# Optimization experiments

Hardware: AMD Instinct MI355X
Metric: run time of the kernel (lower is better)

## Reference

```python
import jax, jax.numpy as jnp
import numpy as np

N_HEAD = 16


def _rope_cos_sin(T, head_dim, dtype):
    inv_freq = 1.0 / (10000.0 ** (jnp.arange(0, head_dim, 2, dtype=jnp.float32) / head_dim))
    t = jnp.arange(T, dtype=jnp.float32)
    freqs = jnp.outer(t, inv_freq)  # [T, head_dim//2]
    return jnp.cos(freqs).astype(dtype), jnp.sin(freqs).astype(dtype)


def _apply_rope(x, cos, sin):
    # x: [B, H, T, D]; cos/sin: [T, D//2]
    x_even = x[..., ::2]
    x_odd = x[..., 1::2]
    c = cos[None, None, :, :]
    s = sin[None, None, :, :]
    out_even = x_even * c - x_odd * s
    out_odd = x_even * s + x_odd * c
    # interleave back: [..., D//2, 2] -> [..., D]
    return jnp.stack((out_even, out_odd), axis=-1).reshape(x.shape)


def setup_inputs() -> dict:
    key = jax.random.key(0)
    k1, k2, k3 = jax.random.split(key, 3)
    B, T, C = 2, 2048, 1024
    x = jax.random.normal(k1, (B, T, C), dtype=jnp.float32)
    w_qkv = jax.random.normal(k2, (C, 3 * C), dtype=jnp.float32) * (1.0 / np.sqrt(C))
    w_proj = jax.random.normal(k3, (C, C), dtype=jnp.float32) * (1.0 / np.sqrt(C))
    b_proj = jnp.zeros((C,), dtype=jnp.float32)
    return {"x": x, "w_qkv": w_qkv, "w_proj": w_proj, "b_proj": b_proj}


def reference(x, w_qkv, w_proj, b_proj):
    B, T, C = x.shape
    H = N_HEAD
    D = C // H
    qkv = x @ w_qkv  # [B, T, 3C]
    q, k, v = jnp.split(qkv, 3, axis=2)
    # [B, T, C] -> [B, H, T, D]
    q = q.reshape(B, T, H, D).transpose(0, 2, 1, 3)
    k = k.reshape(B, T, H, D).transpose(0, 2, 1, 3)
    v = v.reshape(B, T, H, D).transpose(0, 2, 1, 3)
    cos, sin = _rope_cos_sin(T, D, q.dtype)
    q = _apply_rope(q, cos, sin)
    k = _apply_rope(k, cos, sin)
    # causal SDPA
    scale = 1.0 / np.sqrt(D)
    att = jnp.einsum('bhqd,bhkd->bhqk', q, k) * scale
    causal = jnp.tril(jnp.ones((T, T), dtype=bool))
    att = jnp.where(causal[None, None, :, :], att, jnp.finfo(att.dtype).min)
    att = jax.nn.softmax(att, axis=-1)
    y = jnp.einsum('bhqk,bhkd->bhqd', att, v)  # [B, H, T, D]
    y = y.transpose(0, 2, 1, 3).reshape(B, T, C)
    return y @ w_proj + b_proj
```

## Files before the change

### kernel.cpp

```cpp
#include <hip/hip_runtime.h>
#include <math.h>

#define T_SEQ 2048
#define CDIM  1024
#define HEADS 16
#define DHEAD 64
#define BATCH 2
#define M_ROWS 4096
#define QSCALE 0.18033688011112042f

typedef unsigned short u16;
typedef unsigned int u32;
typedef __attribute__((ext_vector_type(8))) short bf16x8;
typedef __attribute__((ext_vector_type(4))) float f32x4;

__device__ inline u16 f2bf(float f) {
    u32 u = __builtin_bit_cast(u32, f);
    u32 r = (u + 0x7fffu + ((u >> 16) & 1u)) >> 16;
    return (u16)r;
}

__device__ inline u32 cvtpk(float lo, float hi) {
    u32 r;
    asm("v_cvt_pk_bf16_f32 %0, %1, %2" : "=v"(r) : "v"(lo), "v"(hi));
    return r;
}

__device__ inline float fexp2(float x) {
#if __has_builtin(__builtin_amdgcn_exp2f)
    return __builtin_amdgcn_exp2f(x);
#else
    float r; asm("v_exp_f32 %0, %1" : "=v"(r) : "v"(x)); return r;
#endif
}

__device__ inline void gload16(const void* g, void* l) {
    __builtin_amdgcn_global_load_lds(
        (const __attribute__((address_space(1))) void*)g,
        (__attribute__((address_space(3))) void*)l, 16, 0, 0);
}

__global__ void rope_table_kernel(float* __restrict__ cosT, float* __restrict__ sinT) {
    int idx = blockIdx.x * blockDim.x + threadIdx.x;
    if (idx >= T_SEQ * 32) return;
    int t = idx >> 5;
    int i = idx & 31;
    float expo = (2.0f * (float)i) / 64.0f;
    float inv = powf(10000.0f, -expo);
    float a = (float)t * inv;
    cosT[idx] = cosf(a);
    sinT[idx] = sinf(a);
}

__global__ __launch_bounds__(256)
void conv_bf16(const float* __restrict__ in, u16* __restrict__ out, int n8) {
    int i = blockIdx.x * blockDim.x + threadIdx.x;
    if (i >= n8) return;
    const float4* p = (const float4*)(in + (size_t)i * 8);
    float4 a = p[0], b = p[1];
    uint4 o;
    o.x = (u32)f2bf(a.x) | ((u32)f2bf(a.y) << 16);
    o.y = (u32)f2bf(a.z) | ((u32)f2bf(a.w) << 16);
    o.z = (u32)f2bf(b.x) | ((u32)f2bf(b.y) << 16);
    o.w = (u32)f2bf(b.z) | ((u32)f2bf(b.w) << 16);
    *(uint4*)(out + (size_t)i * 8) = o;
}

__global__ __launch_bounds__(256)
void convT64(const float* __restrict__ in, u16* __restrict__ out, int K, int N) {
    __shared__ float Ls[64][65];
    const int tid = threadIdx.x;
    const int k0 = blockIdx.y << 6, n0 = blockIdx.x << 6;
    const int r0 = tid >> 4, c4 = (tid & 15) << 2;
#pragma unroll
    for (int p = 0; p < 4; p++) {
        int r = r0 + (p << 4);
        float4 v = *(const float4*)&in[(size_t)(k0 + r) * N + n0 + c4];
        Ls[r][c4 + 0] = v.x; Ls[r][c4 + 1] = v.y;
        Ls[r][c4 + 2] = v.z; Ls[r][c4 + 3] = v.w;
    }
    __syncthreads();
    const int n = tid >> 2, kq = (tid & 3) << 4;
    u32 pk[8];
#pragma unroll
    for (int j = 0; j < 8; j++) {
        float lo = Ls[kq + 2 * j][n], hi = Ls[kq + 2 * j + 1][n];
        pk[j] = (u32)f2bf(lo) | ((u32)f2bf(hi) << 16);
    }
    u32* dst = (u32*)&out[(size_t)(n0 + n) * K + k0 + kq];
    ((uint4*)dst)[0] = make_uint4(pk[0], pk[1], pk[2], pk[3]);
    ((uint4*)dst)[1] = make_uint4(pk[4], pk[5], pk[6], pk[7]);
}

__global__ __launch_bounds__(256)
void transposeV(const u16* __restrict__ in, u16* __restrict__ out) {
    __shared__ u16 Ls[64][72];
    const int tid = threadIdx.x;
    const int bh = blockIdx.y;
    const int t0 = blockIdx.x << 6;
    const u16* src = in + ((size_t)bh << 17) + ((size_t)t0 << 6);
#pragma unroll
    for (int p = 0; p < 2; p++) {
        int L = tid + (p << 8);
        int t = L >> 3, c = L & 7;
        uint4 v = *(const uint4*)&src[(size_t)t * 64 + (c << 3)];
        *(uint4*)&Ls[t][c << 3] = v;
    }
    __syncthreads();
    const int d = tid >> 2, tq = (tid & 3) << 4;
    u32 pk[8];
#pragma unroll
    for (int j = 0; j < 8; j++) {
        u16 lo = Ls[tq + 2 * j][d], hi = Ls[tq + 2 * j + 1][d];
        pk[j] = (u32)lo | ((u32)hi << 16);
    }
    u16* dst = out + ((size_t)bh << 17) + ((size_t)d << 11) + t0 + tq;
    ((uint4*)dst)[0] = make_uint4(pk[0], pk[1], pk[2], pk[3]);
    ((uint4*)dst)[1] = make_uint4(pk[4], pk[5], pk[6], pk[7]);
}

template <int EPI>
__global__ __launch_bounds__(256)
void gemm_bf16(const u16* __restrict__ A, const u16* __restrict__ Bt,
               int N, int K,
               const float* __restrict__ bias, float* __restrict__ outF,
               u16* __restrict__ qOut, u16* __restrict__ kOut, u16* __restrict__ vOut,
               const float* __restrict__ cosT, const float* __restrict__ sinT) {
    __shared__ u16 Alds[2][128 * 32];
    __shared__ u16 Blds[2][128 * 32];
    const int tid = threadIdx.x;
    const int lane = tid & 63;
    const int w = tid >> 6;
    const int wr = w >> 1, wc = w & 1;
    const int g = lane >> 4, l15 = lane & 15;
    const int m0 = blockIdx.y * 128, n0 = blockIdx.x * 128;

    f32x4 acc[4][4];
#pragma unroll
    for (int m = 0; m < 4; m++)
#pragma unroll
        for (int n = 0; n < 4; n++)
#pragma unroll
            for (int e = 0; e < 4; e++) acc[m][n][e] = 0.f;

    int aoff[4], boff[4];
#pragma unroll
    for (int m = 0; m < 4; m++) {
        aoff[m] = ((wr << 6) + (m << 4) + l15) * 64 + (g << 4);
        boff[m] = ((wc << 6) + (m << 4) + l15) * 64 + (g << 4);
    }
    const int rowA0 = tid >> 2, kk0 = (tid & 3) << 3;

#define GSTAGE(BUF, K0)                                                          \
    {                                                                            \
        _Pragma("unroll") for (int pq = 0; pq < 2; pq++) {                       \
            int L = tid + (pq << 8);                                             \
            int row = rowA0 + (pq << 6);                                         \
            gload16(A + (size_t)(m0 + row) * K + (K0) + kk0, &Alds[BUF][0] + L * 8); \
            gload16(Bt + (size_t)(n0 + row) * K + (K0) + kk0, &Blds[BUF][0] + L * 8); \
        }                                                                        \
    }

    GSTAGE(0, 0);
    const int nt = K >> 5;
    int cur = 0;
    for (int t = 0; t < nt; t++) {
        if (t + 1 < nt) {
            GSTAGE(cur ^ 1, ((t + 1) << 5));
            asm volatile("s_waitcnt vmcnt(4)" ::: "memory");
        } else {
            asm volatile("s_waitcnt vmcnt(0)" ::: "memory");
        }
        __builtin_amdgcn_s_barrier();
        asm volatile("" ::: "memory");
        bf16x8 af[4], bfr[4];
#pragma unroll
        for (int m = 0; m < 4; m++) af[m] = *(const bf16x8*)((const char*)&Alds[cur][0] + aoff[m]);
#pragma unroll
        for (int n = 0; n < 4; n++) bfr[n] = *(const bf16x8*)((const char*)&Blds[cur][0] + boff[n]);
#pragma unroll
        for (int m = 0; m < 4; m++)
#pragma unroll
            for (int n = 0; n < 4; n++)
                acc[m][n] = __builtin_amdgcn_mfma_f32_16x16x32_bf16(af[m], bfr[n], acc[m][n], 0, 0, 0);
        asm volatile("" ::: "memory");
        __builtin_amdgcn_s_barrier();
        cur ^= 1;
    }
#undef GSTAGE

    if (EPI == 0) {
        const int sec = n0 >> 10;
#pragma unroll
        for (int m = 0; m < 4; m++) {
#pragma unroll
            for (int j = 0; j < 4; j++) {
                int t = m0 + (wr << 6) + (m << 4) + (g << 2) + j;
                int b = t >> 11, tt = t & 2047;
#pragma unroll
                for (int n = 0; n < 4; n++) {
                    int cc = (n0 + (wc << 6) + (n << 4) + l15) & 1023;
                    int h = cc >> 6, d = cc & 63;
                    float val = acc[m][n][j];
                    float o = val;
                    if (sec < 2) {
                        float partner = __shfl_xor(val, 1);
                        int i0 = d >> 1;
                        float c = cosT[tt * 32 + i0], s = sinT[tt * 32 + i0];
                        o = ((d & 1) == 0) ? (val * c - partner * s)
                                           : (partner * s + val * c);
                        if (sec == 0) o *= QSCALE;
                    }
                    size_t off = (((size_t)((b * 16 + h) * 2048 + tt)) << 6) + d;
                    u16* dst = (sec == 0) ? qOut : ((sec == 1) ? kOut : vOut);
                    dst[off] = f2bf(o);
                }
            }
        }
    } else {
#pragma unroll
        for (int m = 0; m < 4; m++) {
#pragma unroll
            for (int j = 0; j < 4; j++) {
                int t = m0 + (wr << 6) + (m << 4) + (g << 2) + j;
#pragma unroll
                for (int n = 0; n < 4; n++) {
                    int col = n0 + (wc << 6) + (n << 4) + l15;
                    outF[(size_t)t * N + col] = acc[m][n][j] + bias[col];
                }
            }
        }
    }
}

__device__ __forceinline__ void kv_stage(const u16* Kbase, const u16* Vtbase,
                                         u16* Kl, u16* Vl, int tid, int kt) {
#pragma unroll
    for (int pp = 0; pp < 2; pp++) {
        int L = tid + (pp << 8);
        int row = L >> 3, c = L & 7;
        int cg = (c ^ (row & 7)) << 3;
        gload16(Kbase + (((size_t)(kt << 6) + row) << 6) + cg, Kl + L * 8);
        gload16(Vtbase + ((size_t)row << 11) + (kt << 6) + cg, Vl + L * 8);
    }
}

__device__ __forceinline__ void attn_step(
    const bf16x8 (&qf)[2], f32x4 (&OF)[4], float (&MR)[4], float (&LR)[4],
    const char* Kl, const char* Vl, bool diag,
    int w, int g, int l15, const int (&rc)[2][4],
    u16* const (&pw)[4], const u16* prd) {
    f32x4 sf[4];
#pragma unroll
    for (int n = 0; n < 4; n++)
#pragma unroll
        for (int e = 0; e < 4; e++) sf[n][e] = 0.f;
#pragma unroll
    for (int s = 0; s < 2; s++)
#pragma unroll
        for (int n = 0; n < 4; n++) {
            bf16x8 kb = *(const bf16x8*)(Kl + rc[s][n]);
            sf[n] = __builtin_amdgcn_mfma_f32_16x16x32_bf16(qf[s], kb, sf[n], 0, 0, 0);
        }
    if (diag) {
#pragma unroll
        for (int n = 0; n < 4; n++)
#pragma unroll
            for (int j = 0; j < 4; j++)
                if ((n << 4) + l15 > (w << 4) + (g << 2) + j) sf[n][j] = -1e30f;
    }
    float mx[4];
#pragma unroll
    for (int j = 0; j < 4; j++)
        mx[j] = fmaxf(fmaxf(sf[0][j], sf[1][j]), fmaxf(sf[2][j], sf[3][j]));
#pragma unroll
    for (int dd = 1; dd < 16; dd <<= 1)
#pragma unroll
        for (int j = 0; j < 4; j++) mx[j] = fmaxf(mx[j], __shfl_xor(mx[j], dd));
    float dmax = fmaxf(fmaxf(mx[0] - MR[0], mx[1] - MR[1]),
                       fmaxf(mx[2] - MR[2], mx[3] - MR[3]));
    if (__ballot(dmax > 10.f) != 0ull) {
#pragma unroll
        for (int j = 0; j < 4; j++) {
            float nm = fmaxf(MR[j], mx[j]);
            float al = fexp2(MR[j] - nm);
            MR[j] = nm;
            LR[j] *= al;
#pragma unroll
            for (int n = 0; n < 4; n++) OF[n][j] *= al;
        }
    }
    float rs[4] = {0.f, 0.f, 0.f, 0.f};
#pragma unroll
    for (int n = 0; n < 4; n++)
#pragma unroll
        for (int j = 0; j < 4; j++) {
            float pv = fexp2(sf[n][j] - MR[j]);
            sf[n][j] = pv;
            rs[j] += pv;
        }
#pragma unroll
    for (int dd = 1; dd < 16; dd <<= 1)
#pragma unroll
        for (int j = 0; j < 4; j++) rs[j] += __shfl_xor(rs[j], dd);
#pragma unroll
    for (int j = 0; j < 4; j++) LR[j] += rs[j];
#pragma unroll
    for (int n = 0; n < 4; n++) {
        u32 p01 = cvtpk(sf[n][0], sf[n][1]);
        u32 p23 = cvtpk(sf[n][2], sf[n][3]);
        pw[0][n * 16] = (u16)p01; pw[1][n * 16] = (u16)(p01 >> 16);
        pw[2][n * 16] = (u16)p23; pw[3][n * 16] = (u16)(p23 >> 16);
    }
    asm volatile("s_waitcnt lgkmcnt(0)" ::: "memory");
    __builtin_amdgcn_sched_barrier(0);
#pragma unroll
    for (int s = 0; s < 2; s++) {
        bf16x8 pa = *(const bf16x8*)(prd + (s << 5) + (g << 3));
#pragma unroll
        for (int n = 0; n < 4; n++) {
            bf16x8 vb = *(const bf16x8*)(Vl + rc[s][n]);
            OF[n] = __builtin_amdgcn_mfma_f32_16x16x32_bf16(pa, vb, OF[n], 0, 0, 0);
        }
    }
}

__device__ __forceinline__ void attn_store(
    const f32x4 (&OF)[4], const float (&LR)[4], u16* Yg, int b, int h,
    int q0, int w, int g, int l15) {
#pragma unroll
    for (int j = 0; j < 4; j++) {
        float inv = 1.0f / LR[j];
        int t = q0 + (w << 4) + (g << 2) + j;
#pragma unroll
        for (int n = 0; n < 4; n++) {
            int d = (n << 4) + l15;
            Yg[((size_t)(b * 2048 + t) << 10) + (h << 6) + d] = f2bf(OF[n][j] * inv);
        }
    }
}

__global__ __launch_bounds__(256)
void attn_mfma(const u16* __restrict__ Qg, const u16* __restrict__ Kg,
               const u16* __restrict__ Vtg, u16* __restrict__ Yg) {
    __shared__ u16 Ks[2][64 * 64];
    __shared__ u16 Vts[2][64 * 64];
    __shared__ u16 Ps[4][16][72];

    const int tid = threadIdx.x;
    const int lane = tid & 63;
    const int w = tid >> 6;
    const int g = lane >> 4, l15 = lane & 15;
    const int p = blockIdx.x;
    const int bh = blockIdx.y;
    const int b = bh >> 4, h = bh & 15;
    const int qtA = p, qtB = 31 - p;
    const int q0A = qtA << 6, q0B = qtB << 6;

    const u16* Qbase = Qg + ((size_t)bh << 17);
    const u16* Kbase = Kg + ((size_t)bh << 17);
    const u16* Vtbase = Vtg + ((size_t)bh << 17);

    const int qrowL = (w << 4) + l15;
    bf16x8 qfA[2], qfB[2];
#pragma unroll
    for (int s = 0; s < 2; s++) {
        qfA[s] = *(const bf16x8*)(Qbase + ((size_t)(q0A + qrowL) << 6) + (s << 5) + (g << 3));
        qfB[s] = *(const bf16x8*)(Qbase + ((size_t)(q0B + qrowL) << 6) + (s << 5) + (g << 3));
    }

    int rc[2][4];
#pragma unroll
    for (int s = 0; s < 2; s++)
#pragma unroll
        for (int n = 0; n < 4; n++) {
            int row = (n << 4) + l15;
            rc[s][n] = row * 128 + ((((s << 2) + g) ^ (row & 7)) << 4);
        }
    u16* pw[4];
#pragma unroll
    for (int j = 0; j < 4; j++) pw[j] = &Ps[w][(g << 2) + j][l15];
    const u16* prd = &Ps[w][l15][0];

    f32x4 OA[4], OB[4];
    float mA[4], lA[4], mB[4], lB[4];
#pragma unroll
    for (int n = 0; n < 4; n++)
#pragma unroll
        for (int e = 0; e < 4; e++) { OA[n][e] = 0.f; OB[n][e] = 0.f; }
#pragma unroll
    for (int j = 0; j < 4; j++) { mA[j] = -INFINITY; lA[j] = 0.f; mB[j] = -INFINITY; lB[j] = 0.f; }

    kv_stage(Kbase, Vtbase, &Ks[0][0], &Vts[0][0], tid, 0);
    int cur = 0;

    for (int kt = 0; kt <= qtA; kt++) {
        int kvn = (kt < qtA) ? kt + 1 : 0;
        kv_stage(Kbase, Vtbase, &Ks[cur ^ 1][0], &Vts[cur ^ 1][0], tid, kvn);
        asm volatile("s_waitcnt vmcnt(4)" ::: "memory");
        __builtin_amdgcn_s_barrier();
        asm volatile("" ::: "memory");
        attn_step(qfA, OA, mA, lA, (const char*)&Ks[cur][0], (const char*)&Vts[cur][0],
                  kt == qtA, w, g, l15, rc, pw, prd);
        asm volatile("" ::: "memory");
        __builtin_amdgcn_s_barrier();
        cur ^= 1;
    }
    attn_store(OA, lA, Yg, b, h, q0A, w, g, l15);

    for (int kt = 0; kt <= qtB; kt++) {
        if (kt < qtB) {
            kv_stage(Kbase, Vtbase, &Ks[cur ^ 1][0], &Vts[cur ^ 1][0], tid, kt + 1);
            asm volatile("s_waitcnt vmcnt(4)" ::: "memory");
        } else {
            asm volatile("s_waitcnt vmcnt(0)" ::: "memory");
        }
        __builtin_amdgcn_s_barrier();
        asm volatile("" ::: "memory");
        attn_step(qfB, OB, mB, lB, (const char*)&Ks[cur][0], (const char*)&Vts[cur][0],
                  kt == qtB, w, g, l15, rc, pw, prd);
        asm volatile("" ::: "memory");
        __builtin_amdgcn_s_barrier();
        cur ^= 1;
    }
    attn_store(OB, lB, Yg, b, h, q0B, w, g, l15);
}

extern "C" void kernel_launch(void* const* d_in, const int* in_sizes, int n_in,
                              void* d_out, int out_size, void* d_ws, size_t ws_size,
                              hipStream_t stream) {
    const float* x      = (const float*)d_in[0];
    const float* w_qkv  = (const float*)d_in[1];
    const float* w_proj = (const float*)d_in[2];
    const float* b_proj = (const float*)d_in[3];
    float* out = (float*)d_out;

    const size_t SZ = (size_t)M_ROWS * CDIM;
    char* ws = (char*)d_ws;
    u16* xb     = (u16*)ws;                ws += SZ * 2;
    u16* wqkvT  = (u16*)ws;                ws += (size_t)3 * CDIM * CDIM * 2;
    u16* wprojT = (u16*)ws;                ws += (size_t)CDIM * CDIM * 2;
    u16* Qb     = (u16*)ws;                ws += SZ * 2;
    u16* Kb     = (u16*)ws;                ws += SZ * 2;
    u16* Vb     = (u16*)ws;                ws += SZ * 2;
    u16* Vt     = (u16*)ws;                ws += SZ * 2;
    u16* Yb     = (u16*)ws;                ws += SZ * 2;
    float* cosT = (float*)ws;              ws += (size_t)T_SEQ * 32 * 4;
    float* sinT = (float*)ws;              ws += (size_t)T_SEQ * 32 * 4;

    rope_table_kernel<<<dim3(256), dim3(256), 0, stream>>>(cosT, sinT);
    conv_bf16<<<dim3(2048), dim3(256), 0, stream>>>(x, xb, (int)(SZ / 8));
    convT64<<<dim3(48, 16), dim3(256), 0, stream>>>(w_qkv, wqkvT, CDIM, 3 * CDIM);
    convT64<<<dim3(16, 16), dim3(256), 0, stream>>>(w_proj, wprojT, CDIM, CDIM);

    gemm_bf16<0><<<dim3(24, 32), dim3(256), 0, stream>>>(
        xb, wqkvT, 3 * CDIM, CDIM, nullptr, nullptr, Qb, Kb, Vb, cosT, sinT);

    transposeV<<<dim3(32, 32), dim3(256), 0, stream>>>(Vb, Vt);

    attn_mfma<<<dim3(16, 32), dim3(256), 0, stream>>>(Qb, Kb, Vt, Yb);

    gemm_bf16<1><<<dim3(8, 32), dim3(256), 0, stream>>>(
        Yb, wprojT, CDIM, CDIM, b_proj, out, nullptr, nullptr, nullptr, nullptr, nullptr);
}
```

Measured before the change: 228.9 us.

## Rewrite attention with 32x32 MFMA, register-resident P via permlane swap

The flash-attention kernel moves from 16x16x32 MFMA tiles with four waves of 16 query rows to 32x32x16 MFMA tiles with two waves of 32 query rows each (128 threads per block). It computes S transposed (K times Q), so each lane holds one query column. The P matrix is then repacked in registers with v_permlane32_swap instead of round-tripping through a shared-memory staging buffer. The row max and sum reductions shrink to a single cross-half shuffle, and diagonal tiles skip the fully masked 32-key sub-tile on wave 0. The cost is half as many waves per block, which lowers latency hiding, plus heavier register pressure from the f32x16 accumulators.

```diff
diff --git a/kernel.cpp b/kernel.cpp
--- a/kernel.cpp
+++ b/kernel.cpp
@@ -13,6 +13,7 @@
 typedef unsigned int u32;
 typedef __attribute__((ext_vector_type(8))) short bf16x8;
 typedef __attribute__((ext_vector_type(4))) float f32x4;
+typedef __attribute__((ext_vector_type(16))) float f32x16;
 
 __device__ inline u16 f2bf(float f) {
     u32 u = __builtin_bit_cast(u32, f);
@@ -24,6 +25,10 @@
     u32 r;
     asm("v_cvt_pk_bf16_f32 %0, %1, %2" : "=v"(r) : "v"(lo), "v"(hi));
     return r;
+}
+
+__device__ inline void permswap(u32& x, u32& y) {
+    asm volatile("v_permlane32_swap_b32 %0, %1" : "+v"(x), "+v"(y));
 }
 
 __device__ inline float fexp2(float x) {
@@ -233,197 +238,207 @@
     }
 }
 
-__device__ __forceinline__ void kv_stage(const u16* Kbase, const u16* Vtbase,
-                                         u16* Kl, u16* Vl, int tid, int kt) {
-#pragma unroll
-    for (int pp = 0; pp < 2; pp++) {
-        int L = tid + (pp << 8);
+__device__ __forceinline__ void kv_stage2(const u16* Kb, const u16* Vtb,
+                                          u16* Kl, u16* Vl, int tid, int k0) {
+#pragma unroll
+    for (int pp = 0; pp < 4; pp++) {
+        int L = tid + (pp << 7);
         int row = L >> 3, c = L & 7;
         int cg = (c ^ (row & 7)) << 3;
-        gload16(Kbase + (((size_t)(kt << 6) + row) << 6) + cg, Kl + L * 8);
-        gload16(Vtbase + ((size_t)row << 11) + (kt << 6) + cg, Vl + L * 8);
-    }
-}
-
-__device__ __forceinline__ void attn_step(
-    const bf16x8 (&qf)[2], f32x4 (&OF)[4], float (&MR)[4], float (&LR)[4],
-    const char* Kl, const char* Vl, bool diag,
-    int w, int g, int l15, const int (&rc)[2][4],
-    u16* const (&pw)[4], const u16* prd) {
-    f32x4 sf[4];
-#pragma unroll
-    for (int n = 0; n < 4; n++)
-#pragma unroll
-        for (int e = 0; e < 4; e++) sf[n][e] = 0.f;
-#pragma unroll
-    for (int s = 0; s < 2; s++)
-#pragma unroll
-        for (int n = 0; n < 4; n++) {
-            bf16x8 kb = *(const bf16x8*)(Kl + rc[s][n]);
-            sf[n] = __builtin_amdgcn_mfma_f32_16x16x32_bf16(qf[s], kb, sf[n], 0, 0, 0);
-        }
+        gload16(Kb + (((size_t)(k0 + row)) << 6) + cg, Kl + L * 8);
+        gload16(Vtb + ((size_t)row << 11) + k0 + cg, Vl + L * 8);
+    }
+}
+
+template <int NS>
+__device__ __forceinline__ void attn_step32(
+    const bf16x8 (&qf)[4], f32x16 (&O)[2], float& MR, float& LR,
+    const char* Kl, const char* Vl, const int (&foff)[2][4],
+    int lim, bool diag) {
+    f32x16 st[NS];
+#pragma unroll
+    for (int s = 0; s < NS; s++) {
+#pragma unroll
+        for (int e = 0; e < 16; e++) st[s][e] = 0.f;
+#pragma unroll
+        for (int ks = 0; ks < 4; ks++) {
+            bf16x8 kf = *(const bf16x8*)(Kl + foff[s][ks]);
+            st[s] = __builtin_amdgcn_mfma_f32_32x32x16_bf16(kf, qf[ks], st[s], 0, 0, 0);
+        }
+    }
     if (diag) {
 #pragma unroll
-        for (int n = 0; n < 4; n++)
-#pragma unroll
-            for (int j = 0; j < 4; j++)
-                if ((n << 4) + l15 > (w << 4) + (g << 2) + j) sf[n][j] = -1e30f;
-    }
-    float mx[4];
-#pragma unroll
-    for (int j = 0; j < 4; j++)
-        mx[j] = fmaxf(fmaxf(sf[0][j], sf[1][j]), fmaxf(sf[2][j], sf[3][j]));
-#pragma unroll
-    for (int dd = 1; dd < 16; dd <<= 1)
-#pragma unroll
-        for (int j = 0; j < 4; j++) mx[j] = fmaxf(mx[j], __shfl_xor(mx[j], dd));
-    float dmax = fmaxf(fmaxf(mx[0] - MR[0], mx[1] - MR[1]),
-                       fmaxf(mx[2] - MR[2], mx[3] - MR[3]));
-    if (__ballot(dmax > 10.f) != 0ull) {
-#pragma unroll
-        for (int j = 0; j < 4; j++) {
-            float nm = fmaxf(MR[j], mx[j]);
-            float al = fexp2(MR[j] - nm);
-            MR[j] = nm;
-            LR[j] *= al;
-#pragma unroll
-            for (int n = 0; n < 4; n++) OF[n][j] *= al;
-        }
-    }
-    float rs[4] = {0.f, 0.f, 0.f, 0.f};
-#pragma unroll
-    for (int n = 0; n < 4; n++)
-#pragma unroll
-        for (int j = 0; j < 4; j++) {
-            float pv = fexp2(sf[n][j] - MR[j]);
-            sf[n][j] = pv;
-            rs[j] += pv;
-        }
-#pragma unroll
-    for (int dd = 1; dd < 16; dd <<= 1)
-#pragma unroll
-        for (int j = 0; j < 4; j++) rs[j] += __shfl_xor(rs[j], dd);
-#pragma unroll
-    for (int j = 0; j < 4; j++) LR[j] += rs[j];
-#pragma unroll
-    for (int n = 0; n < 4; n++) {
-        u32 p01 = cvtpk(sf[n][0], sf[n][1]);
-        u32 p23 = cvtpk(sf[n][2], sf[n][3]);
-        pw[0][n * 16] = (u16)p01; pw[1][n * 16] = (u16)(p01 >> 16);
-        pw[2][n * 16] = (u16)p23; pw[3][n * 16] = (u16)(p23 >> 16);
-    }
-    asm volatile("s_waitcnt lgkmcnt(0)" ::: "memory");
-    __builtin_amdgcn_sched_barrier(0);
-#pragma unroll
-    for (int s = 0; s < 2; s++) {
-        bf16x8 pa = *(const bf16x8*)(prd + (s << 5) + (g << 3));
-#pragma unroll
-        for (int n = 0; n < 4; n++) {
-            bf16x8 vb = *(const bf16x8*)(Vl + rc[s][n]);
-            OF[n] = __builtin_amdgcn_mfma_f32_16x16x32_bf16(pa, vb, OF[n], 0, 0, 0);
-        }
-    }
-}
-
-__device__ __forceinline__ void attn_store(
-    const f32x4 (&OF)[4], const float (&LR)[4], u16* Yg, int b, int h,
-    int q0, int w, int g, int l15) {
-#pragma unroll
-    for (int j = 0; j < 4; j++) {
-        float inv = 1.0f / LR[j];
-        int t = q0 + (w << 4) + (g << 2) + j;
-#pragma unroll
-        for (int n = 0; n < 4; n++) {
-            int d = (n << 4) + l15;
-            Yg[((size_t)(b * 2048 + t) << 10) + (h << 6) + d] = f2bf(OF[n][j] * inv);
-        }
-    }
-}
-
-__global__ __launch_bounds__(256)
+        for (int r = 0; r < 16; r++) {
+            const int kvloc = (r & 3) + 8 * (r >> 2);
+            if (kvloc > lim) st[NS - 1][r] = -1e30f;
+        }
+    }
+    float t8[8];
+#pragma unroll
+    for (int r = 0; r < 8; r++) {
+        float a = fmaxf(st[0][r], st[0][r + 8]);
+        if (NS == 2) a = fmaxf(a, fmaxf(st[1][r], st[1][r + 8]));
+        t8[r] = a;
+    }
+    float m = fmaxf(fmaxf(fmaxf(t8[0], t8[4]), fmaxf(t8[1], t8[5])),
+                    fmaxf(fmaxf(t8[2], t8[6]), fmaxf(t8[3], t8[7])));
+    m = fmaxf(m, __shfl_xor(m, 32));
+    float mn = fmaxf(MR, m);
+    if (__ballot(m - MR > 10.f)) {
+        float al = fexp2(MR - mn);
+        MR = mn;
+        LR *= al;
+#pragma unroll
+        for (int e = 0; e < 16; e++) { O[0][e] *= al; O[1][e] *= al; }
+    }
+    float s0 = 0.f, s1 = 0.f, s2 = 0.f, s3 = 0.f;
+#pragma unroll
+    for (int s = 0; s < NS; s++)
+#pragma unroll
+        for (int r = 0; r < 16; r++) {
+            float pv = fexp2(st[s][r] - MR);
+            st[s][r] = pv;
+            if ((r & 3) == 0) s0 += pv;
+            else if ((r & 3) == 1) s1 += pv;
+            else if ((r & 3) == 2) s2 += pv;
+            else s3 += pv;
+        }
+    float sum = (s0 + s1) + (s2 + s3);
+    sum += __shfl_xor(sum, 32);
+    LR += sum;
+#pragma unroll
+    for (int ks = 0; ks < 2 * NS; ks++) {
+        const int sT = ks >> 1, b1 = (ks & 1) << 3;
+        u32 a = cvtpk(st[sT][b1 + 0], st[sT][b1 + 1]);
+        u32 b = cvtpk(st[sT][b1 + 2], st[sT][b1 + 3]);
+        u32 c = cvtpk(st[sT][b1 + 4], st[sT][b1 + 5]);
+        u32 d = cvtpk(st[sT][b1 + 6], st[sT][b1 + 7]);
+        permswap(a, c);
+        permswap(b, d);
+        bf16x8 pf = __builtin_bit_cast(bf16x8, make_uint4(a, b, c, d));
+#pragma unroll
+        for (int t2 = 0; t2 < 2; t2++) {
+            bf16x8 vf = *(const bf16x8*)(Vl + foff[t2][ks]);
+            O[t2] = __builtin_amdgcn_mfma_f32_32x32x16_bf16(vf, pf, O[t2], 0, 0, 0);
+        }
+    }
+}
+
+__device__ __forceinline__ void attn_store32(
+    const f32x16 (&O)[2], float LR, u16* __restrict__ Yg,
+    int b, int hd, int q, int hl) {
+    float inv = 1.0f / LR;
+    size_t rowoff = (((size_t)(b * 2048 + q)) << 10) + (hd << 6);
+#pragma unroll
+    for (int t2 = 0; t2 < 2; t2++)
+#pragma unroll
+        for (int rg = 0; rg < 4; rg++) {
+            int d0 = (rg << 3) + (hl << 2) + (t2 << 5);
+            u32 lo = cvtpk(O[t2][4 * rg + 0] * inv, O[t2][4 * rg + 1] * inv);
+            u32 hi = cvtpk(O[t2][4 * rg + 2] * inv, O[t2][4 * rg + 3] * inv);
+            *(uint2*)&Yg[rowoff + d0] = make_uint2(lo, hi);
+        }
+}
+
+__global__ __launch_bounds__(128)
 void attn_mfma(const u16* __restrict__ Qg, const u16* __restrict__ Kg,
                const u16* __restrict__ Vtg, u16* __restrict__ Yg) {
     __shared__ u16 Ks[2][64 * 64];
     __shared__ u16 Vts[2][64 * 64];
-    __shared__ u16 Ps[4][16][72];
 
     const int tid = threadIdx.x;
     const int lane = tid & 63;
     const int w = tid >> 6;
-    const int g = lane >> 4, l15 = lane & 15;
+    const int l31 = lane & 31, hl = lane >> 5;
     const int p = blockIdx.x;
     const int bh = blockIdx.y;
-    const int b = bh >> 4, h = bh & 15;
+    const int b = bh >> 4, hd = bh & 15;
     const int qtA = p, qtB = 31 - p;
-    const int q0A = qtA << 6, q0B = qtB << 6;
-
-    const u16* Qbase = Qg + ((size_t)bh << 17);
-    const u16* Kbase = Kg + ((size_t)bh << 17);
-    const u16* Vtbase = Vtg + ((size_t)bh << 17);
-
-    const int qrowL = (w << 4) + l15;
-    bf16x8 qfA[2], qfB[2];
-#pragma unroll
-    for (int s = 0; s < 2; s++) {
-        qfA[s] = *(const bf16x8*)(Qbase + ((size_t)(q0A + qrowL) << 6) + (s << 5) + (g << 3));
-        qfB[s] = *(const bf16x8*)(Qbase + ((size_t)(q0B + qrowL) << 6) + (s << 5) + (g << 3));
-    }
-
-    int rc[2][4];
+    const int lim = l31 - (hl << 2);
+
+    const u16* Qb = Qg + ((size_t)bh << 17);
+    const u16* Kb = Kg + ((size_t)bh << 17);
+    const u16* Vtb = Vtg + ((size_t)bh << 17);
+
+    int foff[2][4];
 #pragma unroll
     for (int s = 0; s < 2; s++)
 #pragma unroll
-        for (int n = 0; n < 4; n++) {
-            int row = (n << 4) + l15;
-            rc[s][n] = row * 128 + ((((s << 2) + g) ^ (row & 7)) << 4);
-        }
-    u16* pw[4];
-#pragma unroll
-    for (int j = 0; j < 4; j++) pw[j] = &Ps[w][(g << 2) + j][l15];
-    const u16* prd = &Ps[w][l15][0];
-
-    f32x4 OA[4], OB[4];
-    float mA[4], lA[4], mB[4], lB[4];
-#pragma unroll
-    for (int n = 0; n < 4; n++)
-#pragma unroll
-        for (int e = 0; e < 4; e++) { OA[n][e] = 0.f; OB[n][e] = 0.f; }
-#pragma unroll
-    for (int j = 0; j < 4; j++) { mA[j] = -INFINITY; lA[j] = 0.f; mB[j] = -INFINITY; lB[j] = 0.f; }
-
-    kv_stage(Kbase, Vtbase, &Ks[0][0], &Vts[0][0], tid, 0);
+        for (int ks = 0; ks < 4; ks++) {
+            int row = (s << 5) + l31;
+            foff[s][ks] = row * 128 + (((hl + (ks << 1)) ^ (row & 7)) << 4);
+        }
+
+    const int qrA = (qtA << 6) + (w << 5) + l31;
+    const int qrB = (qtB << 6) + (w << 5) + l31;
+    bf16x8 qfA[4], qfB[4];
+#pragma unroll
+    for (int ks = 0; ks < 4; ks++) {
+        int co = (hl << 3) + (ks << 4);
+        qfA[ks] = *(const bf16x8*)(Qb + (((size_t)qrA) << 6) + co);
+        qfB[ks] = *(const bf16x8*)(Qb + (((size_t)qrB) << 6) + co);
+    }
+
+    kv_stage2(Kb, Vtb, &Ks[0][0], &Vts[0][0], tid, 0);
     int cur = 0;
 
+    f32x16 O[2];
+    float MR, LR;
+
+#pragma unroll
+    for (int e = 0; e < 16; e++) { O[0][e] = 0.f; O[1][e] = 0.f; }
+    MR = -1e30f; LR = 0.f;
     for (int kt = 0; kt <= qtA; kt++) {
-        int kvn = (kt < qtA) ? kt + 1 : 0;
-        kv_stage(Kbase, Vtbase, &Ks[cur ^ 1][0], &Vts[cur ^ 1][0], tid, kvn);
-        asm volatile("s_waitcnt vmcnt(4)" ::: "memory");
-        __builtin_amdgcn_s_barrier();
-        asm volatile("" ::: "memory");
-        attn_step(qfA, OA, mA, lA, (const char*)&Ks[cur][0], (const char*)&Vts[cur][0],
-                  kt == qtA, w, g, l15, rc, pw, prd);
+        int nk0 = (kt < qtA) ? ((kt + 1) << 6) : 0;
+        kv_stage2(Kb, Vtb, &Ks[cur ^ 1][0], &Vts[cur ^ 1][0], tid, nk0);
+        asm volatile("s_waitcnt vmcnt(8)" ::: "memory");
+        __builtin_amdgcn_s_barrier();
+        asm volatile("" ::: "memory");
+        if (kt == qtA) {
+            if (w == 0)
+                attn_step32<1>(qfA, O, MR, LR, (const char*)&Ks[cur][0],
+                               (const char*)&Vts[cur][0], foff, lim, true);
+            else
+                attn_step32<2>(qfA, O, MR, LR, (const char*)&Ks[cur][0],
+                               (const char*)&Vts[cur][0], foff, lim, true);
+        } else {
+            attn_step32<2>(qfA, O, MR, LR, (const char*)&Ks[cur][0],
+                           (const char*)&Vts[cur][0], foff, lim, false);
+        }
         asm volatile("" ::: "memory");
         __builtin_amdgcn_s_barrier();
         cur ^= 1;
     }
-    attn_store(OA, lA, Yg, b, h, q0A, w, g, l15);
-
+    attn_store32(O, LR, Yg, b, hd, qrA, hl);
+
+#pragma unroll
+    for (int e = 0; e < 16; e++) { O[0][e] = 0.f; O[1][e] = 0.f; }
+    MR = -1e30f; LR = 0.f;
     for (int kt = 0; kt <= qtB; kt++) {
         if (kt < qtB) {
-            kv_stage(Kbase, Vtbase, &Ks[cur ^ 1][0], &Vts[cur ^ 1][0], tid, kt + 1);
-            asm volatile("s_waitcnt vmcnt(4)" ::: "memory");
+            kv_stage2(Kb, Vtb, &Ks[cur ^ 1][0], &Vts[cur ^ 1][0], tid, (kt + 1) << 6);
+            asm volatile("s_waitcnt vmcnt(8)" ::: "memory");
         } else {
             asm volatile("s_waitcnt vmcnt(0)" ::: "memory");
         }
         __builtin_amdgcn_s_barrier();
         asm volatile("" ::: "memory");
-        attn_step(qfB, OB, mB, lB, (const char*)&Ks[cur][0], (const char*)&Vts[cur][0],
-                  kt == qtB, w, g, l15, rc, pw, prd);
+        if (kt == qtB) {
+            if (w == 0)
+                attn_step32<1>(qfB, O, MR, LR, (const char*)&Ks[cur][0],
+                               (const char*)&Vts[cur][0], foff, lim, true);
+            else
+                attn_step32<2>(qfB, O, MR, LR, (const char*)&Ks[cur][0],
+                               (const char*)&Vts[cur][0], foff, lim, true);
+        } else {
+            attn_step32<2>(qfB, O, MR, LR, (const char*)&Ks[cur][0],
+                           (const char*)&Vts[cur][0], foff, lim, false);
+        }
         asm volatile("" ::: "memory");
         __builtin_amdgcn_s_barrier();
         cur ^= 1;
     }
-    attn_store(OB, lB, Yg, b, h, q0B, w, g, l15);
+    attn_store32(O, LR, Yg, b, hd, qrB, hl);
 }
 
 extern "C" void kernel_launch(void* const* d_in, const int* in_sizes, int n_in,
@@ -458,7 +473,7 @@
 
     transposeV<<<dim3(32, 32), dim3(256), 0, stream>>>(Vb, Vt);
 
-    attn_mfma<<<dim3(16, 32), dim3(256), 0, stream>>>(Qb, Kb, Vt, Yb);
+    attn_mfma<<<dim3(16, 32), dim3(128), 0, stream>>>(Qb, Kb, Vt, Yb);
 
     gemm_bf16<1><<<dim3(8, 32), dim3(256), 0, stream>>>(
         Yb, wprojT, CDIM, CDIM, b_proj, out, nullptr, nullptr, nullptr, nullptr, nullptr);
```

After: 230.2 us. About the same (+0.6%).
